# Performance work log

Measured on AMD Instinct MI355X. Metric: run time of the kernel, lower is better.

## Reference

```python
import jax, jax.numpy as jnp
import numpy as np

N = 50000      # nodes (both x and t sets)
D = 128        # d_hidden
E = 1600000    # edges per edge_index (avg degree 32)
LN_EPS = 1e-5


def _gin(x_src, x_dst, edge, W1, b1, W2, b2):
    # PyG GINConv, eps=0: nn(x_dst + sum_{j->i} x_src[j])
    agg = jax.ops.segment_sum(x_src[edge[0]], edge[1], num_segments=x_dst.shape[0])
    h = x_dst + agg
    h = jax.nn.relu(h @ W1 + b1)
    return h @ W2 + b2


def _layernorm(h, g, b):
    m = jnp.mean(h, axis=-1, keepdims=True)
    v = jnp.var(h, axis=-1, keepdims=True)
    return (h - m) / jnp.sqrt(v + LN_EPS) * g + b


def setup_inputs() -> dict:
    key = jax.random.key(0)
    ks = jax.random.split(key, 24)
    s = 1.0 / np.sqrt(D)
    w = lambda k: (jax.random.uniform(k, (D, D), dtype=jnp.float32) * 2 - 1) * s
    b = lambda k: (jax.random.uniform(k, (D,), dtype=jnp.float32) * 2 - 1) * s
    return {
        "x": jax.random.normal(ks[0], (N, D), dtype=jnp.float32),
        "t": jax.random.normal(ks[1], (N, D), dtype=jnp.float32),
        "e_t": jax.random.randint(ks[2], (2, E), 0, N),
        "e_xct": jax.random.randint(ks[3], (2, E), 0, N),
        # gat_tt GIN MLP
        "W1a": w(ks[4]), "b1a": b(ks[5]), "W2a": w(ks[6]), "b2a": b(ks[7]),
        # gat_xct GIN MLP
        "W1b": w(ks[8]), "b1b": b(ks[9]), "W2b": w(ks[10]), "b2b": b(ks[11]),
        # out: Linear -> ReLU -> LayerNorm
        "Wo": w(ks[12]), "bo": b(ks[13]),
        "ln_g": jnp.ones((D,), dtype=jnp.float32),
        "ln_b": jnp.zeros((D,), dtype=jnp.float32),
        # fc_x: Linear -> ReLU -> Linear
        "Wf1": w(ks[14]), "bf1": b(ks[15]), "Wf2": w(ks[16]), "bf2": b(ks[17]),
    }


def reference(x, t, e_t, e_xct,
              W1a, b1a, W2a, b2a,
              W1b, b1b, W2b, b2b,
              Wo, bo, ln_g, ln_b,
              Wf1, bf1, Wf2, bf2):
    # t = (t + gat_tt(t, e_t) + gat_xct((x, t), e_xct)).relu()
    t2 = jax.nn.relu(t
                     + _gin(t, t, e_t, W1a, b1a, W2a, b2a)
                     + _gin(x, t, e_xct, W1b, b1b, W2b, b2b))
    # out branch: Linear -> ReLU -> LayerNorm, residual add
    t_out = t2 + _layernorm(jax.nn.relu(t2 @ Wo + bo), ln_g, ln_b)
    # fc_x branch: Linear -> ReLU -> Linear, residual add
    x_out = x + (jax.nn.relu(x @ Wf1 + bf1) @ Wf2 + bf2)
    return (x_out, t_out)
```

## Files before the change

kernel.cpp:

```cpp
#include <hip/hip_runtime.h>

#define DD 128
#define BSH 7
#define LSTR 136

typedef __attribute__((ext_vector_type(8))) short bf16x8;
typedef __attribute__((ext_vector_type(4))) float f32x4;
typedef __attribute__((ext_vector_type(2))) float f32x2;

__device__ __forceinline__ unsigned short f2b(float f){
  unsigned u = __builtin_bit_cast(unsigned, f);
  u += 0x7FFFu + ((u >> 16) & 1u);
  return (unsigned short)(u >> 16);
}
__device__ __forceinline__ float blo(unsigned u){ return __builtin_bit_cast(float, u << 16); }
__device__ __forceinline__ float bhi(unsigned u){ return __builtin_bit_cast(float, u & 0xFFFF0000u); }
__device__ __forceinline__ float b2f(unsigned short h){ return __builtin_bit_cast(float, ((unsigned)h) << 16); }
__device__ __forceinline__ unsigned pk2(float a, float b){
  return (unsigned)f2b(a) | ((unsigned)f2b(b) << 16);
}

struct WP { const float* w[7]; };
__global__ __launch_bounds__(256) void k_pre(const float* __restrict__ x,
    const float* __restrict__ t, unsigned* __restrict__ xh, unsigned* __restrict__ th,
    int M, WP p, unsigned short* __restrict__ wt,
    const int* __restrict__ e_t, const int* __restrict__ e_xct,
    int* __restrict__ gbcount, int E, int NBper, int ncv, int N){
  const int bid = blockIdx.x;
  if (bid < ncv){
    int tid = bid*256 + threadIdx.x;
    if (tid < M){
      float4 v = ((const float4*)x)[tid];
      ((uint2*)xh)[tid] = make_uint2(pk2(v.x, v.y), pk2(v.z, v.w));
    } else if (tid < 2*M){
      int k = tid - M;
      float4 v = ((const float4*)t)[k];
      ((uint2*)th)[k] = make_uint2(pk2(v.x, v.y), pk2(v.z, v.w));
    }
    return;
  }
  if (bid < ncv + 7){
    const float* W = p.w[bid - ncv];
    unsigned short* dst = wt + (size_t)(bid - ncv)*DD*DD;
    for (int e = threadIdx.x; e < DD*DD; e += 256){
      int k = e >> 7, c = e & 127;
      dst[(c*DD + k) ^ ((c & 7) << 3)] = f2b(W[e]);
    }
    return;
  }
  if (bid == ncv + 7){
    const int tid = threadIdx.x;
    uint4 z; z.x = 0; z.y = 0; z.z = 0; z.w = 0;
    if (tid < 16)      ((uint4*)(xh + (size_t)N*(DD/2)))[tid]      = z;
    else if (tid < 32) ((uint4*)(th + (size_t)N*(DD/2)))[tid - 16] = z;
    return;
  }
  __shared__ int h[800];
  const int vb = bid - ncv - 8;
  const int NB2 = 2*NBper;
  for (int i = threadIdx.x; i < NB2; i += 256) h[i] = 0;
  __syncthreads();
  const long total = 2L*E;
  for (long idx = (long)vb*256 + threadIdx.x; idx < total; idx += 65536L){
    int s = idx >= E;
    int e = (int)(idx - (s ? (long)E : 0));
    int d = (s ? e_xct : e_t)[E + e];
    atomicAdd(&h[s*NBper + (d >> BSH)], 1);
  }
  __syncthreads();
  for (int i = threadIdx.x; i < NB2; i += 256)
    if (h[i]) atomicAdd(&gbcount[i], h[i]);
}

__global__ void k_bscan(const int* __restrict__ gbcount, int* __restrict__ gbase,
                        int* __restrict__ gcursor, int NB2, int total){
  __shared__ int sm[1024];
  const int t = threadIdx.x;
  int v = (t < NB2) ? gbcount[t] : 0;
  sm[t] = v; __syncthreads();
  for (int d = 1; d < 1024; d <<= 1){
    int u = (t >= d) ? sm[t-d] : 0;
    __syncthreads();
    sm[t] += u;
    __syncthreads();
  }
  if (t < NB2){ int ex = sm[t] - v; gbase[t] = ex; gcursor[t] = ex; }
  if (t == 0) gbase[NB2] = total;
}

#define SCCH 8192
__global__ __launch_bounds__(256) void k_scatter(const int* __restrict__ e_t,
    const int* __restrict__ e_xct, int* __restrict__ gcursor,
    unsigned* __restrict__ gbucket, int E, int NBper){
  __shared__ int cnt[800]; __shared__ int gpos[800]; __shared__ int cur[800];
  const int NB2 = 2*NBper;
  const int t = threadIdx.x;
  for (int i = t; i < NB2; i += 256){ cnt[i] = 0; cur[i] = 0; }
  __syncthreads();
  const long base = (long)blockIdx.x * SCCH;
  const long end  = min(base + SCCH, 2L*E);
  for (long idx = base + t; idx < end; idx += 256){
    int s = idx >= E;
    int e = (int)(idx - (s ? (long)E : 0));
    int d = (s ? e_xct : e_t)[E + e];
    atomicAdd(&cnt[s*NBper + (d >> BSH)], 1);
  }
  __syncthreads();
  for (int i = t; i < NB2; i += 256)
    if (cnt[i]) gpos[i] = atomicAdd(&gcursor[i], cnt[i]);
  __syncthreads();
  for (long idx = base + t; idx < end; idx += 256){
    int s = idx >= E;
    int e = (int)(idx - (s ? (long)E : 0));
    const int* ei = s ? e_xct : e_t;
    int sv = ei[e];
    int d  = ei[E + e];
    int b  = s*NBper + (d >> BSH);
    int pos = atomicAdd(&cur[b], 1);
    gbucket[gpos[b] + pos] = (unsigned)sv | ((unsigned)d << 16);
  }
}

__global__ __launch_bounds__(256) void k_build(const unsigned* __restrict__ gbucket,
    const int* __restrict__ gbase, int* __restrict__ offs,
    unsigned short* __restrict__ csr, int N, int E, int NBper){
  __shared__ int cnt[128]; __shared__ int pre[128]; __shared__ int cur[128];
  const int b  = blockIdx.x;
  const int s  = b >= NBper;
  const int bb = b - s*NBper;
  const int d0 = bb << BSH;
  const int t  = threadIdx.x;
  if (t < 128) cnt[t] = 0;
  __syncthreads();
  const int g0 = gbase[b], g1 = gbase[b+1];
  for (int j = g0 + t; j < g1; j += 256){
    unsigned en = gbucket[j];
    atomicAdd(&cnt[(en >> 16) & 127], 1);
  }
  __syncthreads();
  int v = (t < 128) ? cnt[t] : 0;
  if (t < 128) pre[t] = v;
  __syncthreads();
  for (int d = 1; d < 128; d <<= 1){
    int u = (t >= d && t < 128) ? pre[t-d] : 0;
    __syncthreads();
    if (t < 128) pre[t] += u;
    __syncthreads();
  }
  if (t < 128){
    int ex = pre[t] - v;
    cur[t] = ex;
    int dd = d0 + t;
    if (dd < N) offs[(size_t)s*(N+1) + dd] = (g0 - s*E) + ex;
  }
  if (t == 128 + 0 && bb == NBper-1) offs[(size_t)s*(N+1) + N] = E;
  __syncthreads();
  for (int j = g0 + t; j < g1; j += 256){
    unsigned en = gbucket[j];
    int d7 = (en >> 16) & 127;
    int pos = atomicAdd(&cur[d7], 1);
    csr[(size_t)g0 + pos] = (unsigned short)(en & 0xFFFFu);
  }
}

__global__ __launch_bounds__(256) void k_gather(const unsigned short* __restrict__ th,
    const unsigned short* __restrict__ xh, const int* __restrict__ offs,
    const unsigned short* __restrict__ csr, unsigned short* hA, unsigned short* hB,
    int N, int E){
  const int w = threadIdx.x >> 6, l = threadIdx.x & 63;
  const long wid = (long)blockIdx.x*4 + w;
  if (wid >= 2L*N) return;
  const int s = wid >= N;
  const int i = (int)(wid - (s ? N : 0));
  const int* off = offs + (size_t)s*(N+1);
  const unsigned short* src = s ? xh : th;
  const unsigned short* cs = csr + (size_t)s*E;
  const int o0 = off[i], o1 = off[i+1];
  const int deg = o1 - o0;
  const int rs = l >> 4;
  const int q  = l & 15;
  const unsigned short* srcq = src + q*8;
  f32x2 A0 = 0.f, A1 = 0.f, A2 = 0.f, A3 = 0.f;
  if (deg > 0){
    int ce = cs[o0 + (l < deg ? l : deg-1)];
    for (int base = 0; base < deg; base += 64){
      const int nb = min(64, deg - base);
      const int ce_cur = ce;
      const int nxt = base + 64;
      if (nxt < deg){
        const int rem2 = deg - nxt;
        ce = cs[o0 + nxt + (l < rem2 ? l : rem2-1)];
      }
      for (int jj = 0; jj < nb; jj += 16){
        #pragma unroll
        for (int u4 = 0; u4 < 4; ++u4){
          const int idx = jj + u4*4 + rs;
          int r = __shfl(ce_cur, idx);
          r = (idx < nb) ? r : N;
          uint4 v = *(const uint4*)(srcq + (size_t)r*DD);
          A0 += (f32x2){blo(v.x), bhi(v.x)};
          A1 += (f32x2){blo(v.y), bhi(v.y)};
          A2 += (f32x2){blo(v.z), bhi(v.z)};
          A3 += (f32x2){blo(v.w), bhi(v.w)};
        }
      }
    }
  }
  #pragma unroll
  for (int m = 16; m <= 32; m <<= 1){
    A0.x += __shfl_xor(A0.x, m); A0.y += __shfl_xor(A0.y, m);
    A1.x += __shfl_xor(A1.x, m); A1.y += __shfl_xor(A1.y, m);
    A2.x += __shfl_xor(A2.x, m); A2.y += __shfl_xor(A2.y, m);
    A3.x += __shfl_xor(A3.x, m); A3.y += __shfl_xor(A3.y, m);
  }
  if (l < 16){
    uint4 tv = *(const uint4*)(th + (size_t)i*DD + q*8);
    A0 += (f32x2){blo(tv.x), bhi(tv.x)};
    A1 += (f32x2){blo(tv.y), bhi(tv.y)};
    A2 += (f32x2){blo(tv.z), bhi(tv.z)};
    A3 += (f32x2){blo(tv.w), bhi(tv.w)};
    uint4 o;
    o.x = pk2(A0.x, A0.y); o.y = pk2(A1.x, A1.y);
    o.z = pk2(A2.x, A2.y); o.w = pk2(A3.x, A3.y);
    *(uint4*)((s ? hB : hA) + (size_t)i*DD + q*8) = o;
  }
}


__device__ __forceinline__ void stage_issue(const unsigned short* __restrict__ Wt,
                                            unsigned short* wlds){
  const int tid = threadIdx.x;
  const int w = tid >> 6, l = tid & 63;
  #pragma unroll
  for (int i = 0; i < 8; ++i){
    const int cbase = i*256 + w*64;
    __builtin_amdgcn_global_load_lds(
      (const __attribute__((address_space(1))) unsigned*)(Wt + (size_t)(cbase + l)*8),
      (__attribute__((address_space(3))) unsigned*)(wlds + (size_t)cbase*8),
      16, 0, 0);
  }
}

__device__ __forceinline__ void gemm_reg(const bf16x8 a[4], int c0, int g, int swz,
    const unsigned short* wlds, f32x4 acc[8]){
  #pragma unroll
  for (int kb = 0; kb < 4; ++kb){
    const int co = (kb*32 + g*8) ^ swz;
    #pragma unroll
    for (int cb = 0; cb < 8; ++cb){
      bf16x8 b = *(const bf16x8*)(wlds + (cb*16 + c0)*DD + co);
      acc[cb] = __builtin_amdgcn_mfma_f32_16x16x32_bf16(a[kb], b, acc[cb], 0, 0, 0);
    }
  }
}

__device__ __forceinline__ void gemm_lds(const unsigned short* lds,
    int w, int c0, int g, int swz, const unsigned short* wlds, f32x4 acc[8]){
  const unsigned short* ap = lds + (w*16 + c0)*LSTR + g*8;
  #pragma unroll
  for (int kb = 0; kb < 4; ++kb){
    bf16x8 a = *(const bf16x8*)(ap + kb*32);
    const int co = (kb*32 + g*8) ^ swz;
    #pragma unroll
    for (int cb = 0; cb < 8; ++cb){
      bf16x8 b = *(const bf16x8*)(wlds + (cb*16 + c0)*DD + co);
      acc[cb] = __builtin_amdgcn_mfma_f32_16x16x32_bf16(a, b, acc[cb], 0, 0, 0);
    }
  }
}

__device__ __forceinline__ void chainT_body(unsigned short* lds, unsigned short* wlds,
    int bid,
    const unsigned short* __restrict__ hA, const unsigned short* __restrict__ hB,
    const unsigned short* __restrict__ W1a, const float* __restrict__ b1a,
    const unsigned short* __restrict__ W2a, const float* __restrict__ b2a,
    const unsigned short* __restrict__ W1b, const float* __restrict__ b1b,
    const unsigned short* __restrict__ W2b, const float* __restrict__ b2b,
    const unsigned short* __restrict__ Wo,  const float* __restrict__ bo,
    const unsigned short* __restrict__ th,
    const float* __restrict__ lng, const float* __restrict__ lnb,
    float* __restrict__ outT, int N)
{
  const int tid = threadIdx.x;
  const int w = tid >> 6, l = tid & 63;
  const int g = l >> 4, c0 = l & 15;
  const int swz = (c0 & 7) << 3;
  const int rbase = bid*64 + w*16;

  int arow = rbase + c0; if (arow > N-1) arow = N-1;
  const unsigned short* apA = hA + (size_t)arow*DD + g*8;
  const unsigned short* apB = hB + (size_t)arow*DD + g*8;
  bf16x8 aA[4], aB[4];
  #pragma unroll
  for (int kb = 0; kb < 4; ++kb){
    aA[kb] = *(const bf16x8*)(apA + kb*32);
    aB[kb] = *(const bf16x8*)(apB + kb*32);
  }
  unsigned short thr_[8][4];
  #pragma unroll
  for (int cb = 0; cb < 8; ++cb){
    #pragma unroll
    for (int r = 0; r < 4; ++r){
      int orow = rbase + 4*g + r;
      int rc = orow > N-1 ? N-1 : orow;
      thr_[cb][r] = th[(size_t)rc*DD + cb*16 + c0];
    }
  }
  stage_issue(W1a, wlds);
  __syncthreads();

  f32x4 acc[8];

  #pragma unroll
  for (int cb = 0; cb < 8; ++cb) acc[cb] = 0.f;
  gemm_reg(aA, c0, g, swz, wlds, acc);
  __syncthreads();
  stage_issue(W2a, wlds);
  #pragma unroll
  for (int cb = 0; cb < 8; ++cb){
    float bv = b1a[cb*16 + c0];
    #pragma unroll
    for (int r = 0; r < 4; ++r)
      lds[(w*16 + 4*g + r)*LSTR + cb*16 + c0] = f2b(fmaxf(acc[cb][r] + bv, 0.f));
  }
  __syncthreads();

  #pragma unroll
  for (int cb = 0; cb < 8; ++cb) acc[cb] = 0.f;
  gemm_lds(lds, w, c0, g, swz, wlds, acc);
  float pAv[8][4];
  #pragma unroll
  for (int cb = 0; cb < 8; ++cb){
    float bv = b2a[cb*16 + c0];
    #pragma unroll
    for (int r = 0; r < 4; ++r) pAv[cb][r] = acc[cb][r] + bv;
  }
  __syncthreads();
  stage_issue(W1b, wlds);
  __syncthreads();

  #pragma unroll
  for (int cb = 0; cb < 8; ++cb) acc[cb] = 0.f;
  gemm_reg(aB, c0, g, swz, wlds, acc);
  __syncthreads();
  stage_issue(W2b, wlds);
  #pragma unroll
  for (int cb = 0; cb < 8; ++cb){
    float bv = b1b[cb*16 + c0];
    #pragma unroll
    for (int r = 0; r < 4; ++r)
      lds[(w*16 + 4*g + r)*LSTR + cb*16 + c0] = f2b(fmaxf(acc[cb][r] + bv, 0.f));
  }
  __syncthreads();

  #pragma unroll
  for (int cb = 0; cb < 8; ++cb) acc[cb] = 0.f;
  gemm_lds(lds, w, c0, g, swz, wlds, acc);
  __syncthreads();
  stage_issue(Wo, wlds);

  float t2f[8][4];
  #pragma unroll
  for (int cb = 0; cb < 8; ++cb){
    float bv = b2b[cb*16 + c0];
    #pragma unroll
    for (int r = 0; r < 4; ++r){
      float v = fmaxf(acc[cb][r] + bv + b2f(thr_[cb][r]) + pAv[cb][r], 0.f);
      t2f[cb][r] = v;
      lds[(w*16 + 4*g + r)*LSTR + cb*16 + c0] = f2b(v);
    }
  }
  __syncthreads();

  #pragma unroll
  for (int cb = 0; cb < 8; ++cb) acc[cb] = 0.f;
  gemm_lds(lds, w, c0, g, swz, wlds, acc);

  float u[8][4];
  float sm_[4] = {0,0,0,0}, sq_[4] = {0,0,0,0};
  #pragma unroll
  for (int cb = 0; cb < 8; ++cb){
    float bv = bo[cb*16 + c0];
    #pragma unroll
    for (int r = 0; r < 4; ++r){
      float v = fmaxf(acc[cb][r] + bv, 0.f);
      u[cb][r] = v;
      sm_[r] += v; sq_[r] += v*v;
    }
  }
  #pragma unroll
  for (int m = 1; m < 16; m <<= 1){
    #pragma unroll
    for (int r = 0; r < 4; ++r){
      sm_[r] += __shfl_xor(sm_[r], m, 64);
      sq_[r] += __shfl_xor(sq_[r], m, 64);
    }
  }
  float mean[4], rstd[4];
  #pragma unroll
  for (int r = 0; r < 4; ++r){
    mean[r] = sm_[r] * (1.0f/DD);
    float var = sq_[r] * (1.0f/DD) - mean[r]*mean[r];
    rstd[r] = rsqrtf(var + 1e-5f);
  }
  #pragma unroll
  for (int cb = 0; cb < 8; ++cb){
    float gv = lng[cb*16 + c0], bv2 = lnb[cb*16 + c0];
    #pragma unroll
    for (int r = 0; r < 4; ++r){
      int orow = rbase + 4*g + r;
      if (orow < N){
        size_t oi = (size_t)orow*DD + cb*16 + c0;
        outT[oi] = (u[cb][r] - mean[r]) * rstd[r] * gv + bv2 + t2f[cb][r];
      }
    }
  }
}

__device__ __forceinline__ void mlp2_body(unsigned short* lds, unsigned short* wlds,
    int bid,
    const unsigned short* __restrict__ X,
    const unsigned short* __restrict__ W1, const float* __restrict__ b1,
    const unsigned short* __restrict__ W2, const float* __restrict__ b2,
    const unsigned short* __restrict__ resh, float* __restrict__ outF, int N)
{
  const int tid = threadIdx.x;
  const int w = tid >> 6, l = tid & 63;
  const int g = l >> 4, c0 = l & 15;
  const int swz = (c0 & 7) << 3;
  const int rbase = bid*64 + w*16;

  int arow = rbase + c0; if (arow > N-1) arow = N-1;
  const unsigned short* apX = X + (size_t)arow*DD + g*8;
  bf16x8 aX[4];
  #pragma unroll
  for (int kb = 0; kb < 4; ++kb) aX[kb] = *(const bf16x8*)(apX + kb*32);
  unsigned short rs_[8][4];
  #pragma unroll
  for (int cb = 0; cb < 8; ++cb){
    #pragma unroll
    for (int r = 0; r < 4; ++r){
      int orow = rbase + 4*g + r;
      int rc = orow > N-1 ? N-1 : orow;
      rs_[cb][r] = resh[(size_t)rc*DD + cb*16 + c0];
    }
  }
  stage_issue(W1, wlds);
  __syncthreads();

  f32x4 acc[8];
  #pragma unroll
  for (int cb = 0; cb < 8; ++cb) acc[cb] = 0.f;
  gemm_reg(aX, c0, g, swz, wlds, acc);
  __syncthreads();
  stage_issue(W2, wlds);
  #pragma unroll
  for (int cb = 0; cb < 8; ++cb){
    float bv = b1[cb*16 + c0];
    #pragma unroll
    for (int r = 0; r < 4; ++r)
      lds[(w*16 + 4*g + r)*LSTR + cb*16 + c0] = f2b(fmaxf(acc[cb][r] + bv, 0.f));
  }
  __syncthreads();

  #pragma unroll
  for (int cb = 0; cb < 8; ++cb) acc[cb] = 0.f;
  gemm_lds(lds, w, c0, g, swz, wlds, acc);

  #pragma unroll
  for (int cb = 0; cb < 8; ++cb){
    float bv = b2[cb*16 + c0];
    #pragma unroll
    for (int r = 0; r < 4; ++r){
      int orow = rbase + 4*g + r;
      if (orow < N){
        size_t oi = (size_t)orow*DD + cb*16 + c0;
        outF[oi] = acc[cb][r] + bv + b2f(rs_[cb][r]);
      }
    }
  }
}

__global__ __launch_bounds__(256, 3) void k_tail(
    const unsigned short* __restrict__ hA, const unsigned short* __restrict__ hB,
    const unsigned short* __restrict__ xh, const unsigned short* __restrict__ th,
    const unsigned short* __restrict__ wt,
    const float* __restrict__ b1a, const float* __restrict__ b2a,
    const float* __restrict__ b1b, const float* __restrict__ b2b,
    const float* __restrict__ bo,  const float* __restrict__ lng,
    const float* __restrict__ lnb, const float* __restrict__ bf1,
    const float* __restrict__ bf2,
    float* __restrict__ outX, float* __restrict__ outT, int N, int gg)
{
  __shared__ unsigned short lds[64*LSTR];
  __shared__ unsigned short wlds[DD*DD];
  const unsigned short* W1a = wt + 0*DD*DD;
  const unsigned short* W2a = wt + 1*DD*DD;
  const unsigned short* W1b = wt + 2*DD*DD;
  const unsigned short* W2b = wt + 3*DD*DD;
  const unsigned short* Wo  = wt + 4*DD*DD;
  const unsigned short* Wf1 = wt + 5*DD*DD;
  const unsigned short* Wf2 = wt + 6*DD*DD;
  if (blockIdx.x < (unsigned)gg){
    chainT_body(lds, wlds, blockIdx.x, hA, hB, W1a, b1a, W2a, b2a, W1b, b1b, W2b, b2b,
                Wo, bo, th, lng, lnb, outT, N);
  } else {
    mlp2_body(lds, wlds, blockIdx.x - gg, xh, Wf1, bf1, Wf2, bf2, xh, outX, N);
  }
}

extern "C" void kernel_launch(void* const* d_in, const int* in_sizes, int n_in,
                              void* d_out, int out_size, void* d_ws, size_t ws_size,
                              hipStream_t stream) {
  const float* x     = (const float*)d_in[0];
  const float* t     = (const float*)d_in[1];
  const int*   e_t   = (const int*)d_in[2];
  const int*   e_xct = (const int*)d_in[3];
  const float* b1a = (const float*)d_in[5];
  const float* b2a = (const float*)d_in[7];
  const float* b1b = (const float*)d_in[9];
  const float* b2b = (const float*)d_in[11];
  const float* bo  = (const float*)d_in[13];
  const float* lng = (const float*)d_in[14];
  const float* lnb = (const float*)d_in[15];
  const float* bf1 = (const float*)d_in[17];
  const float* bf2 = (const float*)d_in[19];

  const int N = in_sizes[0] / DD;
  const int E = in_sizes[2] / 2;
  const int NBper = (N + 127) >> BSH;
  const int NB2 = 2*NBper;

  char* p = (char*)d_ws;
  auto carve = [&](size_t b)->char*{ char* r = p; p += (b + 255) & ~(size_t)255; return r; };
  size_t nd2z = (size_t)(N+1)*DD*2;
  size_t nd2 = (size_t)N*DD*2, nd4 = (size_t)N*DD*4;
  unsigned short* xh = (unsigned short*)carve(nd2z);
  unsigned short* th = (unsigned short*)carve(nd2z);
  unsigned short* hA = (unsigned short*)carve(nd2);
  unsigned short* hB = (unsigned short*)carve(nd2);
  float*          pA = (float*)carve(nd4);
  unsigned short* wt = (unsigned short*)carve((size_t)7*DD*DD*2);
  int* gbcount = (int*)carve((size_t)NB2*4);
  int* gbase   = (int*)carve((size_t)(NB2+1)*4);
  int* gcursor = (int*)carve((size_t)NB2*4);
  int* offs    = (int*)carve((size_t)2*(N+1)*4);
  unsigned short* csr = (unsigned short*)carve((size_t)2*E*2);
  unsigned* gbucket = (unsigned*)pA;

  float* outX = (float*)d_out;
  float* outT = outX + (size_t)N*DD;

  hipMemsetAsync(gbcount, 0, (size_t)NB2*4, stream);

  WP wp;
  wp.w[0] = (const float*)d_in[4];  wp.w[1] = (const float*)d_in[6];
  wp.w[2] = (const float*)d_in[8];  wp.w[3] = (const float*)d_in[10];
  wp.w[4] = (const float*)d_in[12]; wp.w[5] = (const float*)d_in[16];
  wp.w[6] = (const float*)d_in[18];

  const int M4 = N*DD/4;
  const int ncv = (2*M4 + 255)/256;
  k_pre<<<ncv + 8 + 256, 256, 0, stream>>>(x, t, (unsigned*)xh, (unsigned*)th, M4,
                                           wp, wt, e_t, e_xct, gbcount, E, NBper, ncv, N);
  k_bscan<<<1, 1024, 0, stream>>>(gbcount, gbase, gcursor, NB2, 2*E);
  const int nsc = (int)((2L*E + SCCH-1) / SCCH);
  k_scatter<<<nsc, 256, 0, stream>>>(e_t, e_xct, gcursor, gbucket, E, NBper);
  k_build<<<NB2, 256, 0, stream>>>(gbucket, gbase, offs, csr, N, E, NBper);
  k_gather<<<(2*N + 3)/4, 256, 0, stream>>>(th, xh, offs, csr, hA, hB, N, E);

  const int gg = (N + 63)/64;
  k_tail<<<2*gg, 256, 0, stream>>>(hA, hB, xh, th, wt, b1a, b2a, b1b, b2b, bo,
                                   lng, lnb, bf1, bf2, outX, outT, N, gg);
}
```

Baseline: 232.8 us.

## Build CSR with per-node global atomics histogram and direct scatter

Replaces the two-level bucketed CSR construction (bucket histogram, bucket scatter, per-bucket local sort) with a per-destination global atomic histogram, a three-kernel multi-block prefix scan, and a direct atomic scatter of source indices into CSR positions. This removes the intermediate bucket buffer and one pass over edges. It trades that for heavy global atomic contention: 3.2M global atomics in the histogram and again in the scatter. CSR order within a node becomes nondeterministic, which may affect gather locality.

Result: slower. 583.8 us (+150.8%).

```diff
diff --git a/kernel.cpp b/kernel.cpp
--- a/kernel.cpp
+++ b/kernel.cpp
@@ -1,7 +1,6 @@
 #include <hip/hip_runtime.h>
 
 #define DD 128
-#define BSH 7
 #define LSTR 136
 
 typedef __attribute__((ext_vector_type(8))) short bf16x8;
@@ -25,7 +24,7 @@
     const float* __restrict__ t, unsigned* __restrict__ xh, unsigned* __restrict__ th,
     int M, WP p, unsigned short* __restrict__ wt,
     const int* __restrict__ e_t, const int* __restrict__ e_xct,
-    int* __restrict__ gbcount, int E, int NBper, int ncv, int N){
+    int* __restrict__ ghist, int E, int ncv, int N){
   const int bid = blockIdx.x;
   if (bid < ncv){
     int tid = bid*256 + threadIdx.x;
@@ -55,28 +54,22 @@
     else if (tid < 32) ((uint4*)(th + (size_t)N*(DD/2)))[tid - 16] = z;
     return;
   }
-  __shared__ int h[800];
   const int vb = bid - ncv - 8;
-  const int NB2 = 2*NBper;
-  for (int i = threadIdx.x; i < NB2; i += 256) h[i] = 0;
-  __syncthreads();
   const long total = 2L*E;
   for (long idx = (long)vb*256 + threadIdx.x; idx < total; idx += 65536L){
     int s = idx >= E;
     int e = (int)(idx - (s ? (long)E : 0));
     int d = (s ? e_xct : e_t)[E + e];
-    atomicAdd(&h[s*NBper + (d >> BSH)], 1);
-  }
-  __syncthreads();
-  for (int i = threadIdx.x; i < NB2; i += 256)
-    if (h[i]) atomicAdd(&gbcount[i], h[i]);
-}
-
-__global__ void k_bscan(const int* __restrict__ gbcount, int* __restrict__ gbase,
-                        int* __restrict__ gcursor, int NB2, int total){
+    atomicAdd(&ghist[s*N + d], 1);
+  }
+}
+
+__global__ __launch_bounds__(1024) void k_scan1(int* __restrict__ g,
+    int* __restrict__ bsum, int n){
   __shared__ int sm[1024];
   const int t = threadIdx.x;
-  int v = (t < NB2) ? gbcount[t] : 0;
+  const int i = blockIdx.x*1024 + t;
+  int v = (i < n) ? g[i] : 0;
   sm[t] = v; __syncthreads();
   for (int d = 1; d < 1024; d <<= 1){
     int u = (t >= d) ? sm[t-d] : 0;
@@ -84,83 +77,51 @@
     sm[t] += u;
     __syncthreads();
   }
-  if (t < NB2){ int ex = sm[t] - v; gbase[t] = ex; gcursor[t] = ex; }
-  if (t == 0) gbase[NB2] = total;
-}
-
-#define SCCH 8192
-__global__ __launch_bounds__(256) void k_scatter(const int* __restrict__ e_t,
+  if (i < n) g[i] = sm[t] - v;
+  if (t == 1023) bsum[blockIdx.x] = sm[t];
+}
+
+__global__ void k_scan2(int* __restrict__ bsum, int nb){
+  __shared__ int sm[128];
+  const int t = threadIdx.x;
+  int v = (t < nb) ? bsum[t] : 0;
+  sm[t] = v; __syncthreads();
+  for (int d = 1; d < 128; d <<= 1){
+    int u = (t >= d) ? sm[t-d] : 0;
+    __syncthreads();
+    sm[t] += u;
+    __syncthreads();
+  }
+  if (t < nb) bsum[t] = sm[t] - v;
+}
+
+__global__ __launch_bounds__(1024) void k_scan3(const int* __restrict__ g,
+    const int* __restrict__ bsum, int* __restrict__ gcursor,
+    int* __restrict__ offs, int N, int E){
+  const int j = blockIdx.x*1024 + threadIdx.x;
+  const int n = 2*N;
+  if (j < n){
+    int val = g[j] + bsum[blockIdx.x];
+    gcursor[j] = val;
+    int s = j >= N;
+    int d = j - s*N;
+    offs[s*(N+1) + d] = val - s*E;
+  }
+  if (j == 0){ offs[N] = E; offs[2*N + 1] = E; }
+}
+
+__global__ __launch_bounds__(256) void k_scat2(const int* __restrict__ e_t,
     const int* __restrict__ e_xct, int* __restrict__ gcursor,
-    unsigned* __restrict__ gbucket, int E, int NBper){
-  __shared__ int cnt[800]; __shared__ int gpos[800]; __shared__ int cur[800];
-  const int NB2 = 2*NBper;
-  const int t = threadIdx.x;
-  for (int i = t; i < NB2; i += 256){ cnt[i] = 0; cur[i] = 0; }
-  __syncthreads();
-  const long base = (long)blockIdx.x * SCCH;
-  const long end  = min(base + SCCH, 2L*E);
-  for (long idx = base + t; idx < end; idx += 256){
-    int s = idx >= E;
-    int e = (int)(idx - (s ? (long)E : 0));
-    int d = (s ? e_xct : e_t)[E + e];
-    atomicAdd(&cnt[s*NBper + (d >> BSH)], 1);
-  }
-  __syncthreads();
-  for (int i = t; i < NB2; i += 256)
-    if (cnt[i]) gpos[i] = atomicAdd(&gcursor[i], cnt[i]);
-  __syncthreads();
-  for (long idx = base + t; idx < end; idx += 256){
-    int s = idx >= E;
-    int e = (int)(idx - (s ? (long)E : 0));
-    const int* ei = s ? e_xct : e_t;
-    int sv = ei[e];
-    int d  = ei[E + e];
-    int b  = s*NBper + (d >> BSH);
-    int pos = atomicAdd(&cur[b], 1);
-    gbucket[gpos[b] + pos] = (unsigned)sv | ((unsigned)d << 16);
-  }
-}
-
-__global__ __launch_bounds__(256) void k_build(const unsigned* __restrict__ gbucket,
-    const int* __restrict__ gbase, int* __restrict__ offs,
-    unsigned short* __restrict__ csr, int N, int E, int NBper){
-  __shared__ int cnt[128]; __shared__ int pre[128]; __shared__ int cur[128];
-  const int b  = blockIdx.x;
-  const int s  = b >= NBper;
-  const int bb = b - s*NBper;
-  const int d0 = bb << BSH;
-  const int t  = threadIdx.x;
-  if (t < 128) cnt[t] = 0;
-  __syncthreads();
-  const int g0 = gbase[b], g1 = gbase[b+1];
-  for (int j = g0 + t; j < g1; j += 256){
-    unsigned en = gbucket[j];
-    atomicAdd(&cnt[(en >> 16) & 127], 1);
-  }
-  __syncthreads();
-  int v = (t < 128) ? cnt[t] : 0;
-  if (t < 128) pre[t] = v;
-  __syncthreads();
-  for (int d = 1; d < 128; d <<= 1){
-    int u = (t >= d && t < 128) ? pre[t-d] : 0;
-    __syncthreads();
-    if (t < 128) pre[t] += u;
-    __syncthreads();
-  }
-  if (t < 128){
-    int ex = pre[t] - v;
-    cur[t] = ex;
-    int dd = d0 + t;
-    if (dd < N) offs[(size_t)s*(N+1) + dd] = (g0 - s*E) + ex;
-  }
-  if (t == 128 + 0 && bb == NBper-1) offs[(size_t)s*(N+1) + N] = E;
-  __syncthreads();
-  for (int j = g0 + t; j < g1; j += 256){
-    unsigned en = gbucket[j];
-    int d7 = (en >> 16) & 127;
-    int pos = atomicAdd(&cur[d7], 1);
-    csr[(size_t)g0 + pos] = (unsigned short)(en & 0xFFFFu);
-  }
+    unsigned short* __restrict__ csr, int E, int N){
+  const long idx = (long)blockIdx.x*256 + threadIdx.x;
+  if (idx >= 2L*E) return;
+  const int s = idx >= E;
+  const int e = (int)(idx - (s ? (long)E : 0));
+  const int* ei = s ? e_xct : e_t;
+  int src = ei[e];
+  int dst = ei[E + e];
+  int pos = atomicAdd(&gcursor[s*N + dst], 1);
+  csr[(size_t)pos] = (unsigned short)src;
 }
 
 __global__ __launch_bounds__(256) void k_gather(const unsigned short* __restrict__ th,
@@ -528,30 +489,26 @@
 
   const int N = in_sizes[0] / DD;
   const int E = in_sizes[2] / 2;
-  const int NBper = (N + 127) >> BSH;
-  const int NB2 = 2*NBper;
 
   char* p = (char*)d_ws;
   auto carve = [&](size_t b)->char*{ char* r = p; p += (b + 255) & ~(size_t)255; return r; };
   size_t nd2z = (size_t)(N+1)*DD*2;
-  size_t nd2 = (size_t)N*DD*2, nd4 = (size_t)N*DD*4;
+  size_t nd2 = (size_t)N*DD*2;
   unsigned short* xh = (unsigned short*)carve(nd2z);
   unsigned short* th = (unsigned short*)carve(nd2z);
   unsigned short* hA = (unsigned short*)carve(nd2);
   unsigned short* hB = (unsigned short*)carve(nd2);
-  float*          pA = (float*)carve(nd4);
   unsigned short* wt = (unsigned short*)carve((size_t)7*DD*DD*2);
-  int* gbcount = (int*)carve((size_t)NB2*4);
-  int* gbase   = (int*)carve((size_t)(NB2+1)*4);
-  int* gcursor = (int*)carve((size_t)NB2*4);
+  int* ghist   = (int*)carve((size_t)2*N*4);
+  int* bsum    = (int*)carve((size_t)128*4);
+  int* gcursor = (int*)carve((size_t)2*N*4);
   int* offs    = (int*)carve((size_t)2*(N+1)*4);
   unsigned short* csr = (unsigned short*)carve((size_t)2*E*2);
-  unsigned* gbucket = (unsigned*)pA;
 
   float* outX = (float*)d_out;
   float* outT = outX + (size_t)N*DD;
 
-  hipMemsetAsync(gbcount, 0, (size_t)NB2*4, stream);
+  hipMemsetAsync(ghist, 0, (size_t)2*N*4, stream);
 
   WP wp;
   wp.w[0] = (const float*)d_in[4];  wp.w[1] = (const float*)d_in[6];
@@ -562,11 +519,14 @@
   const int M4 = N*DD/4;
   const int ncv = (2*M4 + 255)/256;
   k_pre<<<ncv + 8 + 256, 256, 0, stream>>>(x, t, (unsigned*)xh, (unsigned*)th, M4,
-                                           wp, wt, e_t, e_xct, gbcount, E, NBper, ncv, N);
-  k_bscan<<<1, 1024, 0, stream>>>(gbcount, gbase, gcursor, NB2, 2*E);
-  const int nsc = (int)((2L*E + SCCH-1) / SCCH);
-  k_scatter<<<nsc, 256, 0, stream>>>(e_t, e_xct, gcursor, gbucket, E, NBper);
-  k_build<<<NB2, 256, 0, stream>>>(gbucket, gbase, offs, csr, N, E, NBper);
+                                           wp, wt, e_t, e_xct, ghist, E, ncv, N);
+  const int n2 = 2*N;
+  const int nblk = (n2 + 1023)/1024;
+  k_scan1<<<nblk, 1024, 0, stream>>>(ghist, bsum, n2);
+  k_scan2<<<1, 128, 0, stream>>>(bsum, nblk);
+  k_scan3<<<nblk, 1024, 0, stream>>>(ghist, bsum, gcursor, offs, N, E);
+  const int nsc = (int)((2L*E + 255) / 256);
+  k_scat2<<<nsc, 256, 0, stream>>>(e_t, e_xct, gcursor, csr, E, N);
   k_gather<<<(2*N + 3)/4, 256, 0, stream>>>(th, xh, offs, csr, hA, hB, N, E);
 
   const int gg = (N + 63)/64;
```

## Move fc_x MLP branch into gather kernel to overlap with edge aggregation

Applied to the files above, without the earlier changes.

The independent x-branch MLP (Linear-ReLU-Linear plus residual) is taken out of the tail kernel and run as extra leading blocks of the gather kernel. Those blocks read the pre-swizzled bf16 weights straight from global memory instead of staging them in LDS. The aim is to hide the small compute-bound GEMM work behind the latency-bound neighbour gather and to shrink the tail kernel to the t-branch only. In exchange, every gather block now reserves a 64x136 bf16 LDS buffer and the kernel gets a `launch_bounds(256,4)` occupancy hint. Weight reads from global may also be slower than reads from LDS.

Result: slower. 254.2 us (+9.2%).

```diff
diff --git a/kernel.cpp b/kernel.cpp
--- a/kernel.cpp
+++ b/kernel.cpp
@@ -163,12 +163,102 @@
   }
 }
 
-__global__ __launch_bounds__(256) void k_gather(const unsigned short* __restrict__ th,
+__device__ __forceinline__ void gemm_reg(const bf16x8 a[4], int c0, int g, int swz,
+    const unsigned short* wimg, f32x4 acc[8]){
+  #pragma unroll
+  for (int kb = 0; kb < 4; ++kb){
+    const int co = (kb*32 + g*8) ^ swz;
+    #pragma unroll
+    for (int cb = 0; cb < 8; ++cb){
+      bf16x8 b = *(const bf16x8*)(wimg + (size_t)(cb*16 + c0)*DD + co);
+      acc[cb] = __builtin_amdgcn_mfma_f32_16x16x32_bf16(a[kb], b, acc[cb], 0, 0, 0);
+    }
+  }
+}
+
+__device__ __forceinline__ void gemm_lds(const unsigned short* lds,
+    int w, int c0, int g, int swz, const unsigned short* wimg, f32x4 acc[8]){
+  const unsigned short* ap = lds + (w*16 + c0)*LSTR + g*8;
+  #pragma unroll
+  for (int kb = 0; kb < 4; ++kb){
+    bf16x8 a = *(const bf16x8*)(ap + kb*32);
+    const int co = (kb*32 + g*8) ^ swz;
+    #pragma unroll
+    for (int cb = 0; cb < 8; ++cb){
+      bf16x8 b = *(const bf16x8*)(wimg + (size_t)(cb*16 + c0)*DD + co);
+      acc[cb] = __builtin_amdgcn_mfma_f32_16x16x32_bf16(a, b, acc[cb], 0, 0, 0);
+    }
+  }
+}
+
+__global__ __launch_bounds__(256, 4) void k_gather(const unsigned short* __restrict__ th,
     const unsigned short* __restrict__ xh, const int* __restrict__ offs,
     const unsigned short* __restrict__ csr, unsigned short* hA, unsigned short* hB,
-    int N, int E){
+    const unsigned short* __restrict__ wt,
+    const float* __restrict__ bf1, const float* __restrict__ bf2,
+    float* __restrict__ outX,
+    int N, int E, int gg){
+  __shared__ unsigned short lds[64*LSTR];
+  if (blockIdx.x < (unsigned)gg){
+    const int bid = blockIdx.x;
+    const int tid = threadIdx.x;
+    const int w = tid >> 6, l = tid & 63;
+    const int g = l >> 4, c0 = l & 15;
+    const int swz = (c0 & 7) << 3;
+    const int rbase = bid*64 + w*16;
+    const unsigned short* Wf1 = wt + 5*DD*DD;
+    const unsigned short* Wf2 = wt + 6*DD*DD;
+
+    int arow = rbase + c0; if (arow > N-1) arow = N-1;
+    const unsigned short* apX = xh + (size_t)arow*DD + g*8;
+    bf16x8 aX[4];
+    #pragma unroll
+    for (int kb = 0; kb < 4; ++kb) aX[kb] = *(const bf16x8*)(apX + kb*32);
+    unsigned short rs_[8][4];
+    #pragma unroll
+    for (int cb = 0; cb < 8; ++cb){
+      #pragma unroll
+      for (int r = 0; r < 4; ++r){
+        int orow = rbase + 4*g + r;
+        int rc = orow > N-1 ? N-1 : orow;
+        rs_[cb][r] = xh[(size_t)rc*DD + cb*16 + c0];
+      }
+    }
+
+    f32x4 acc[8];
+    #pragma unroll
+    for (int cb = 0; cb < 8; ++cb) acc[cb] = 0.f;
+    gemm_reg(aX, c0, g, swz, Wf1, acc);
+
+    #pragma unroll
+    for (int cb = 0; cb < 8; ++cb){
+      float bv = bf1[cb*16 + c0];
+      #pragma unroll
+      for (int r = 0; r < 4; ++r)
+        lds[(w*16 + 4*g + r)*LSTR + cb*16 + c0] = f2b(fmaxf(acc[cb][r] + bv, 0.f));
+    }
+    __syncthreads();
+
+    #pragma unroll
+    for (int cb = 0; cb < 8; ++cb) acc[cb] = 0.f;
+    gemm_lds(lds, w, c0, g, swz, Wf2, acc);
+
+    #pragma unroll
+    for (int cb = 0; cb < 8; ++cb){
+      float bv = bf2[cb*16 + c0];
+      #pragma unroll
+      for (int r = 0; r < 4; ++r){
+        int orow = rbase + 4*g + r;
+        if (orow < N){
+          size_t oi = (size_t)orow*DD + cb*16 + c0;
+          outX[oi] = acc[cb][r] + bv + b2f(rs_[cb][r]);
+        }
+      }
+    }
+    return;
+  }
   const int w = threadIdx.x >> 6, l = threadIdx.x & 63;
-  const long wid = (long)blockIdx.x*4 + w;
+  const long wid = (long)(blockIdx.x - gg)*4 + w;
   if (wid >= 2L*N) return;
   const int s = wid >= N;
   const int i = (int)(wid - (s ? N : 0));
@@ -226,7 +316,6 @@
   }
 }
 
-
 __device__ __forceinline__ void stage_issue(const unsigned short* __restrict__ Wt,
                                             unsigned short* wlds){
   const int tid = threadIdx.x;
@@ -241,256 +330,15 @@
   }
 }
 
-__device__ __forceinline__ void gemm_reg(const bf16x8 a[4], int c0, int g, int swz,
-    const unsigned short* wlds, f32x4 acc[8]){
-  #pragma unroll
-  for (int kb = 0; kb < 4; ++kb){
-    const int co = (kb*32 + g*8) ^ swz;
-    #pragma unroll
-    for (int cb = 0; cb < 8; ++cb){
-      bf16x8 b = *(const bf16x8*)(wlds + (cb*16 + c0)*DD + co);
-      acc[cb] = __builtin_amdgcn_mfma_f32_16x16x32_bf16(a[kb], b, acc[cb], 0, 0, 0);
-    }
-  }
-}
-
-__device__ __forceinline__ void gemm_lds(const unsigned short* lds,
-    int w, int c0, int g, int swz, const unsigned short* wlds, f32x4 acc[8]){
-  const unsigned short* ap = lds + (w*16 + c0)*LSTR + g*8;
-  #pragma unroll
-  for (int kb = 0; kb < 4; ++kb){
-    bf16x8 a = *(const bf16x8*)(ap + kb*32);
-    const int co = (kb*32 + g*8) ^ swz;
-    #pragma unroll
-    for (int cb = 0; cb < 8; ++cb){
-      bf16x8 b = *(const bf16x8*)(wlds + (cb*16 + c0)*DD + co);
-      acc[cb] = __builtin_amdgcn_mfma_f32_16x16x32_bf16(a, b, acc[cb], 0, 0, 0);
-    }
-  }
-}
-
-__device__ __forceinline__ void chainT_body(unsigned short* lds, unsigned short* wlds,
-    int bid,
-    const unsigned short* __restrict__ hA, const unsigned short* __restrict__ hB,
-    const unsigned short* __restrict__ W1a, const float* __restrict__ b1a,
-    const unsigned short* __restrict__ W2a, const float* __restrict__ b2a,
-    const unsigned short* __restrict__ W1b, const float* __restrict__ b1b,
-    const unsigned short* __restrict__ W2b, const float* __restrict__ b2b,
-    const unsigned short* __restrict__ Wo,  const float* __restrict__ bo,
-    const unsigned short* __restrict__ th,
-    const float* __restrict__ lng, const float* __restrict__ lnb,
-    float* __restrict__ outT, int N)
-{
-  const int tid = threadIdx.x;
-  const int w = tid >> 6, l = tid & 63;
-  const int g = l >> 4, c0 = l & 15;
-  const int swz = (c0 & 7) << 3;
-  const int rbase = bid*64 + w*16;
-
-  int arow = rbase + c0; if (arow > N-1) arow = N-1;
-  const unsigned short* apA = hA + (size_t)arow*DD + g*8;
-  const unsigned short* apB = hB + (size_t)arow*DD + g*8;
-  bf16x8 aA[4], aB[4];
-  #pragma unroll
-  for (int kb = 0; kb < 4; ++kb){
-    aA[kb] = *(const bf16x8*)(apA + kb*32);
-    aB[kb] = *(const bf16x8*)(apB + kb*32);
-  }
-  unsigned short thr_[8][4];
-  #pragma unroll
-  for (int cb = 0; cb < 8; ++cb){
-    #pragma unroll
-    for (int r = 0; r < 4; ++r){
-      int orow = rbase + 4*g + r;
-      int rc = orow > N-1 ? N-1 : orow;
-      thr_[cb][r] = th[(size_t)rc*DD + cb*16 + c0];
-    }
-  }
-  stage_issue(W1a, wlds);
-  __syncthreads();
-
-  f32x4 acc[8];
-
-  #pragma unroll
-  for (int cb = 0; cb < 8; ++cb) acc[cb] = 0.f;
-  gemm_reg(aA, c0, g, swz, wlds, acc);
-  __syncthreads();
-  stage_issue(W2a, wlds);
-  #pragma unroll
-  for (int cb = 0; cb < 8; ++cb){
-    float bv = b1a[cb*16 + c0];
-    #pragma unroll
-    for (int r = 0; r < 4; ++r)
-      lds[(w*16 + 4*g + r)*LSTR + cb*16 + c0] = f2b(fmaxf(acc[cb][r] + bv, 0.f));
-  }
-  __syncthreads();
-
-  #pragma unroll
-  for (int cb = 0; cb < 8; ++cb) acc[cb] = 0.f;
-  gemm_lds(lds, w, c0, g, swz, wlds, acc);
-  float pAv[8][4];
-  #pragma unroll
-  for (int cb = 0; cb < 8; ++cb){
-    float bv = b2a[cb*16 + c0];
-    #pragma unroll
-    for (int r = 0; r < 4; ++r) pAv[cb][r] = acc[cb][r] + bv;
-  }
-  __syncthreads();
-  stage_issue(W1b, wlds);
-  __syncthreads();
-
-  #pragma unroll
-  for (int cb = 0; cb < 8; ++cb) acc[cb] = 0.f;
-  gemm_reg(aB, c0, g, swz, wlds, acc);
-  __syncthreads();
-  stage_issue(W2b, wlds);
-  #pragma unroll
-  for (int cb = 0; cb < 8; ++cb){
-    float bv = b1b[cb*16 + c0];
-    #pragma unroll
-    for (int r = 0; r < 4; ++r)
-      lds[(w*16 + 4*g + r)*LSTR + cb*16 + c0] = f2b(fmaxf(acc[cb][r] + bv, 0.f));
-  }
-  __syncthreads();
-
-  #pragma unroll
-  for (int cb = 0; cb < 8; ++cb) acc[cb] = 0.f;
-  gemm_lds(lds, w, c0, g, swz, wlds, acc);
-  __syncthreads();
-  stage_issue(Wo, wlds);
-
-  float t2f[8][4];
-  #pragma unroll
-  for (int cb = 0; cb < 8; ++cb){
-    float bv = b2b[cb*16 + c0];
-    #pragma unroll
-    for (int r = 0; r < 4; ++r){
-      float v = fmaxf(acc[cb][r] + bv + b2f(thr_[cb][r]) + pAv[cb][r], 0.f);
-      t2f[cb][r] = v;
-      lds[(w*16 + 4*g + r)*LSTR + cb*16 + c0] = f2b(v);
-    }
-  }
-  __syncthreads();
-
-  #pragma unroll
-  for (int cb = 0; cb < 8; ++cb) acc[cb] = 0.f;
-  gemm_lds(lds, w, c0, g, swz, wlds, acc);
-
-  float u[8][4];
-  float sm_[4] = {0,0,0,0}, sq_[4] = {0,0,0,0};
-  #pragma unroll
-  for (int cb = 0; cb < 8; ++cb){
-    float bv = bo[cb*16 + c0];
-    #pragma unroll
-    for (int r = 0; r < 4; ++r){
-      float v = fmaxf(acc[cb][r] + bv, 0.f);
-      u[cb][r] = v;
-      sm_[r] += v; sq_[r] += v*v;
-    }
-  }
-  #pragma unroll
-  for (int m = 1; m < 16; m <<= 1){
-    #pragma unroll
-    for (int r = 0; r < 4; ++r){
-      sm_[r] += __shfl_xor(sm_[r], m, 64);
-      sq_[r] += __shfl_xor(sq_[r], m, 64);
-    }
-  }
-  float mean[4], rstd[4];
-  #pragma unroll
-  for (int r = 0; r < 4; ++r){
-    mean[r] = sm_[r] * (1.0f/DD);
-    float var = sq_[r] * (1.0f/DD) - mean[r]*mean[r];
-    rstd[r] = rsqrtf(var + 1e-5f);
-  }
-  #pragma unroll
-  for (int cb = 0; cb < 8; ++cb){
-    float gv = lng[cb*16 + c0], bv2 = lnb[cb*16 + c0];
-    #pragma unroll
-    for (int r = 0; r < 4; ++r){
-      int orow = rbase + 4*g + r;
-      if (orow < N){
-        size_t oi = (size_t)orow*DD + cb*16 + c0;
-        outT[oi] = (u[cb][r] - mean[r]) * rstd[r] * gv + bv2 + t2f[cb][r];
-      }
-    }
-  }
-}
-
-__device__ __forceinline__ void mlp2_body(unsigned short* lds, unsigned short* wlds,
-    int bid,
-    const unsigned short* __restrict__ X,
-    const unsigned short* __restrict__ W1, const float* __restrict__ b1,
-    const unsigned short* __restrict__ W2, const float* __restrict__ b2,
-    const unsigned short* __restrict__ resh, float* __restrict__ outF, int N)
-{
-  const int tid = threadIdx.x;
-  const int w = tid >> 6, l = tid & 63;
-  const int g = l >> 4, c0 = l & 15;
-  const int swz = (c0 & 7) << 3;
-  const int rbase = bid*64 + w*16;
-
-  int arow = rbase + c0; if (arow > N-1) arow = N-1;
-  const unsigned short* apX = X + (size_t)arow*DD + g*8;
-  bf16x8 aX[4];
-  #pragma unroll
-  for (int kb = 0; kb < 4; ++kb) aX[kb] = *(const bf16x8*)(apX + kb*32);
-  unsigned short rs_[8][4];
-  #pragma unroll
-  for (int cb = 0; cb < 8; ++cb){
-    #pragma unroll
-    for (int r = 0; r < 4; ++r){
-      int orow = rbase + 4*g + r;
-      int rc = orow > N-1 ? N-1 : orow;
-      rs_[cb][r] = resh[(size_t)rc*DD + cb*16 + c0];
-    }
-  }
-  stage_issue(W1, wlds);
-  __syncthreads();
-
-  f32x4 acc[8];
-  #pragma unroll
-  for (int cb = 0; cb < 8; ++cb) acc[cb] = 0.f;
-  gemm_reg(aX, c0, g, swz, wlds, acc);
-  __syncthreads();
-  stage_issue(W2, wlds);
-  #pragma unroll
-  for (int cb = 0; cb < 8; ++cb){
-    float bv = b1[cb*16 + c0];
-    #pragma unroll
-    for (int r = 0; r < 4; ++r)
-      lds[(w*16 + 4*g + r)*LSTR + cb*16 + c0] = f2b(fmaxf(acc[cb][r] + bv, 0.f));
-  }
-  __syncthreads();
-
-  #pragma unroll
-  for (int cb = 0; cb < 8; ++cb) acc[cb] = 0.f;
-  gemm_lds(lds, w, c0, g, swz, wlds, acc);
-
-  #pragma unroll
-  for (int cb = 0; cb < 8; ++cb){
-    float bv = b2[cb*16 + c0];
-    #pragma unroll
-    for (int r = 0; r < 4; ++r){
-      int orow = rbase + 4*g + r;
-      if (orow < N){
-        size_t oi = (size_t)orow*DD + cb*16 + c0;
-        outF[oi] = acc[cb][r] + bv + b2f(rs_[cb][r]);
-      }
-    }
-  }
-}
-
 __global__ __launch_bounds__(256, 3) void k_tail(
     const unsigned short* __restrict__ hA, const unsigned short* __restrict__ hB,
-    const unsigned short* __restrict__ xh, const unsigned short* __restrict__ th,
+    const unsigned short* __restrict__ th,
     const unsigned short* __restrict__ wt,
     const float* __restrict__ b1a, const float* __restrict__ b2a,
     const float* __restrict__ b1b, const float* __restrict__ b2b,
     const float* __restrict__ bo,  const float* __restrict__ lng,
-    const float* __restrict__ lnb, const float* __restrict__ bf1,
-    const float* __restrict__ bf2,
-    float* __restrict__ outX, float* __restrict__ outT, int N, int gg)
+    const float* __restrict__ lnb,
+    float* __restrict__ outT, int N)
 {
   __shared__ unsigned short lds[64*LSTR];
   __shared__ unsigned short wlds[DD*DD];
@@ -499,13 +347,141 @@
   const unsigned short* W1b = wt + 2*DD*DD;
   const unsigned short* W2b = wt + 3*DD*DD;
   const unsigned short* Wo  = wt + 4*DD*DD;
-  const unsigned short* Wf1 = wt + 5*DD*DD;
-  const unsigned short* Wf2 = wt + 6*DD*DD;
-  if (blockIdx.x < (unsigned)gg){
-    chainT_body(lds, wlds, blockIdx.x, hA, hB, W1a, b1a, W2a, b2a, W1b, b1b, W2b, b2b,
-                Wo, bo, th, lng, lnb, outT, N);
-  } else {
-    mlp2_body(lds, wlds, blockIdx.x - gg, xh, Wf1, bf1, Wf2, bf2, xh, outX, N);
+
+  const int bid = blockIdx.x;
+  const int tid = threadIdx.x;
+  const int w = tid >> 6, l = tid & 63;
+  const int g = l >> 4, c0 = l & 15;
+  const int swz = (c0 & 7) << 3;
+  const int rbase = bid*64 + w*16;
+
+  int arow = rbase + c0; if (arow > N-1) arow = N-1;
+  const unsigned short* apA = hA + (size_t)arow*DD + g*8;
+  const unsigned short* apB = hB + (size_t)arow*DD + g*8;
+  bf16x8 aA[4], aB[4];
+  #pragma unroll
+  for (int kb = 0; kb < 4; ++kb){
+    aA[kb] = *(const bf16x8*)(apA + kb*32);
+    aB[kb] = *(const bf16x8*)(apB + kb*32);
+  }
+  unsigned short thr_[8][4];
+  #pragma unroll
+  for (int cb = 0; cb < 8; ++cb){
+    #pragma unroll
+    for (int r = 0; r < 4; ++r){
+      int orow = rbase + 4*g + r;
+      int rc = orow > N-1 ? N-1 : orow;
+      thr_[cb][r] = th[(size_t)rc*DD + cb*16 + c0];
+    }
+  }
+  stage_issue(W1a, wlds);
+  __syncthreads();
+
+  f32x4 acc[8];
+
+  #pragma unroll
+  for (int cb = 0; cb < 8; ++cb) acc[cb] = 0.f;
+  gemm_reg(aA, c0, g, swz, wlds, acc);
+  __syncthreads();
+  stage_issue(W2a, wlds);
+  #pragma unroll
+  for (int cb = 0; cb < 8; ++cb){
+    float bv = b1a[cb*16 + c0];
+    #pragma unroll
+    for (int r = 0; r < 4; ++r)
+      lds[(w*16 + 4*g + r)*LSTR + cb*16 + c0] = f2b(fmaxf(acc[cb][r] + bv, 0.f));
+  }
+  __syncthreads();
+
+  #pragma unroll
+  for (int cb = 0; cb < 8; ++cb) acc[cb] = 0.f;
+  gemm_lds(lds, w, c0, g, swz, wlds, acc);
+  float pAv[8][4];
+  #pragma unroll
+  for (int cb = 0; cb < 8; ++cb){
+    float bv = b2a[cb*16 + c0];
+    #pragma unroll
+    for (int r = 0; r < 4; ++r) pAv[cb][r] = acc[cb][r] + bv;
+  }
+  __syncthreads();
+  stage_issue(W1b, wlds);
+  __syncthreads();
+
+  #pragma unroll
+  for (int cb = 0; cb < 8; ++cb) acc[cb] = 0.f;
+  gemm_reg(aB, c0, g, swz, wlds, acc);
+  __syncthreads();
+  stage_issue(W2b, wlds);
+  #pragma unroll
+  for (int cb = 0; cb < 8; ++cb){
+    float bv = b1b[cb*16 + c0];
+    #pragma unroll
+    for (int r = 0; r < 4; ++r)
+      lds[(w*16 + 4*g + r)*LSTR + cb*16 + c0] = f2b(fmaxf(acc[cb][r] + bv, 0.f));
+  }
+  __syncthreads();
+
+  #pragma unroll
+  for (int cb = 0; cb < 8; ++cb) acc[cb] = 0.f;
+  gemm_lds(lds, w, c0, g, swz, wlds, acc);
+  __syncthreads();
+  stage_issue(Wo, wlds);
+
+  float t2f[8][4];
+  #pragma unroll
+  for (int cb = 0; cb < 8; ++cb){
+    float bv = b2b[cb*16 + c0];
+    #pragma unroll
+    for (int r = 0; r < 4; ++r){
+      float v = fmaxf(acc[cb][r] + bv + b2f(thr_[cb][r]) + pAv[cb][r], 0.f);
+      t2f[cb][r] = v;
+      lds[(w*16 + 4*g + r)*LSTR + cb*16 + c0] = f2b(v);
+    }
+  }
+  __syncthreads();
+
+  #pragma unroll
+  for (int cb = 0; cb < 8; ++cb) acc[cb] = 0.f;
+  gemm_lds(lds, w, c0, g, swz, wlds, acc);
+
+  float u[8][4];
+  float sm_[4] = {0,0,0,0}, sq_[4] = {0,0,0,0};
+  #pragma unroll
+  for (int cb = 0; cb < 8; ++cb){
+    float bv = bo[cb*16 + c0];
+    #pragma unroll
+    for (int r = 0; r < 4; ++r){
+      float v = fmaxf(acc[cb][r] + bv, 0.f);
+      u[cb][r] = v;
+      sm_[r] += v; sq_[r] += v*v;
+    }
+  }
+  #pragma unroll
+  for (int m = 1; m < 16; m <<= 1){
+    #pragma unroll
+    for (int r = 0; r < 4; ++r){
+      sm_[r] += __shfl_xor(sm_[r], m, 64);
+      sq_[r] += __shfl_xor(sq_[r], m, 64);
+    }
+  }
+  float mean[4], rstd[4];
+  #pragma unroll
+  for (int r = 0; r < 4; ++r){
+    mean[r] = sm_[r] * (1.0f/DD);
+    float var = sq_[r] * (1.0f/DD) - mean[r]*mean[r];
+    rstd[r] = rsqrtf(var + 1e-5f);
+  }
+  #pragma unroll
+  for (int cb = 0; cb < 8; ++cb){
+    float gv = lng[cb*16 + c0], bv2 = lnb[cb*16 + c0];
+    #pragma unroll
+    for (int r = 0; r < 4; ++r){
+      int orow = rbase + 4*g + r;
+      if (orow < N){
+        size_t oi = (size_t)orow*DD + cb*16 + c0;
+        outT[oi] = (u[cb][r] - mean[r]) * rstd[r] * gv + bv2 + t2f[cb][r];
+      }
+    }
   }
 }
 
@@ -567,9 +543,12 @@
   const int nsc = (int)((2L*E + SCCH-1) / SCCH);
   k_scatter<<<nsc, 256, 0, stream>>>(e_t, e_xct, gcursor, gbucket, E, NBper);
   k_build<<<NB2, 256, 0, stream>>>(gbucket, gbase, offs, csr, N, E, NBper);
-  k_gather<<<(2*N + 3)/4, 256, 0, stream>>>(th, xh, offs, csr, hA, hB, N, E);
 
   const int gg = (N + 63)/64;
-  k_tail<<<2*gg, 256, 0, stream>>>(hA, hB, xh, th, wt, b1a, b2a, b1b, b2b, bo,
-                                   lng, lnb, bf1, bf2, outX, outT, N, gg);
-}
+  const int ngb = (2*N + 3)/4;
+  k_gather<<<gg + ngb, 256, 0, stream>>>(th, xh, offs, csr, hA, hB,
+                                         wt, bf1, bf2, outX, N, E, gg);
+
+  k_tail<<<gg, 256, 0, stream>>>(hA, hB, th, wt, b1a, b2a, b1b, b2b, bo,
+                                 lng, lnb, outT, N);
+}
```
